# Kernel optimization log

Measured on AMD Instinct MI355X. Metric: run time of the kernel, lower is better.

## Reference

```python
import jax, jax.numpy as jnp
import numpy as np

N_NODES = 50000
N_EDGES = 800000
IN_DIM = 256
HID_DIM = 128
N_LAYERS = 3


def setup_inputs() -> dict:
    key = jax.random.key(0)
    ks = jax.random.split(key, 7)
    s = 0.05
    x = jax.random.normal(ks[0], (N_NODES, IN_DIM), dtype=jnp.float32)
    edge_index = jax.random.randint(ks[1], (2, N_EDGES), 0, N_NODES, dtype=jnp.int64)
    W_enc = jax.random.normal(ks[2], (HID_DIM, IN_DIM), dtype=jnp.float32) * s
    b_enc = jax.random.normal(ks[3], (HID_DIM,), dtype=jnp.float32) * s
    W_l = jax.random.normal(ks[4], (N_LAYERS, HID_DIM, HID_DIM), dtype=jnp.float32) * s
    b_l = jax.random.normal(ks[5], (N_LAYERS, HID_DIM), dtype=jnp.float32) * s
    W_r = jax.random.normal(ks[6], (N_LAYERS, HID_DIM, HID_DIM), dtype=jnp.float32) * s
    return {"x": x, "edge_index": edge_index, "W_enc": W_enc, "b_enc": b_enc,
            "W_l": W_l, "b_l": b_l, "W_r": W_r}


def reference(x, edge_index, W_enc, b_enc, W_l, b_l, W_r):
    # eval mode: dropout is identity
    n = x.shape[0]
    src, dst = edge_index[0], edge_index[1]
    # encode: Linear(in_dim -> hid_dim)
    h = x @ W_enc.T + b_enc  # [N, H]
    # in-degree for mean aggregation (nodes with no in-edges -> 0 output)
    deg = jax.ops.segment_sum(jnp.ones((src.shape[0],), h.dtype), dst, num_segments=n)
    denom = jnp.maximum(deg, 1.0)[:, None]  # [N, 1]
    for i in range(W_l.shape[0]):
        # mean of source-node features over incoming edges
        agg = jax.ops.segment_sum(h[src], dst, num_segments=n) / denom  # [N, H]
        # SAGEConv: lin_l(agg) + lin_r(h)  (lin_r has no bias)
        h = agg @ W_l[i].T + b_l[i] + h @ W_r[i].T
    return h
```

## Files before the change

kernel.cpp:

```cpp
#include <hip/hip_runtime.h>

#define N_NODES 50000
#define N_EDGES 800000
#define IN_DIM 256
#define HID_DIM 128
#define ROWTILES 3125
#define ENC_BLOCKS 1024
#define WCVT_BLOCKS 48
#define CNT_BLOCKS 256
#define EDGES_PER_CB 3125
#define NBLK_LAYER 768
#define CAP_E 352
#define TPAD 3136

typedef float f4 __attribute__((ext_vector_type(4)));
typedef float f32x4 __attribute__((ext_vector_type(4)));
typedef float vf2 __attribute__((ext_vector_type(2)));
typedef short bf16x8 __attribute__((ext_vector_type(8)));

__device__ __forceinline__ unsigned short f2bf(float f) {
    unsigned u = __builtin_bit_cast(unsigned, f);
    return (unsigned short)((u + 0x7fffu + ((u >> 16) & 1u)) >> 16);
}
__device__ __forceinline__ unsigned pk2(float a, float b) {
    return (unsigned)f2bf(a) | ((unsigned)f2bf(b) << 16);
}
__device__ __forceinline__ bf16x8 cvt8(f4 a, f4 b) {
    union { bf16x8 v; unsigned u[4]; } r;
    r.u[0] = pk2(a[0], a[1]);
    r.u[1] = pk2(a[2], a[3]);
    r.u[2] = pk2(b[0], b[1]);
    r.u[3] = pk2(b[2], b[3]);
    return r.v;
}
__device__ __forceinline__ vf2 dec8(unsigned short t) {
    return __builtin_amdgcn_cvt_pk_f32_fp8((int)(unsigned)t, false);
}
__device__ __forceinline__ void gl_lds16(const void* g, void* l) {
    __builtin_amdgcn_global_load_lds(
        (const __attribute__((address_space(1))) unsigned int*)g,
        (__attribute__((address_space(3))) unsigned int*)l, 16, 0, 0);
}


__global__ __launch_bounds__(256) void k_pre(const int* __restrict__ dst,
                                             int* __restrict__ Cm,
                                             const float* __restrict__ Wl, const float* __restrict__ Wr,
                                             unsigned short* __restrict__ wlrbf,
                                             const float* __restrict__ x,
                                             const float* __restrict__ Wenc,
                                             const float* __restrict__ bias,
                                             unsigned short* __restrict__ hout,
                                             unsigned char* __restrict__ f8out) {
    __shared__ int smem_i[8192];
    int tid = threadIdx.x;
    if (blockIdx.x < WCVT_BLOCKS) {
        int idx = blockIdx.x * 2048 + tid * 8;
        const float* srcp = (idx < 49152) ? (Wl + idx) : (Wr + (idx - 49152));
        const f4* g = (const f4*)srcp;
        *(bf16x8*)(wlrbf + idx) = cvt8(g[0], g[1]);
        return;
    }
    if (blockIdx.x >= WCVT_BLOCKS + ENC_BLOCKS) {
        int c = blockIdx.x - WCVT_BLOCKS - ENC_BLOCKS;
        int* cnt = smem_i;
        for (int i = tid; i < TPAD; i += 256) cnt[i] = 0;
        __syncthreads();
        const int* dp = dst + c * EDGES_PER_CB;
        for (int i = tid; i < EDGES_PER_CB; i += 256)
            atomicAdd(&cnt[dp[i] >> 4], 1);
        __syncthreads();
        int* crow = Cm + (size_t)c * TPAD;
        for (int t = tid; t < TPAD; t += 256) crow[t] = cnt[t];
        return;
    }
    float* xsf = (float*)smem_i;
    int bid = blockIdx.x - WCVT_BLOCKS;
    int lane = tid & 63;
    int wv = tid >> 6;
    int colbase = wv * 32;
    int lr = lane & 15;
    int kh = (lane >> 4) * 8;
    int khB = kh * 4;
    int swz = (lr & 7) << 4;

    bf16x8 bfr[2][8];
#pragma unroll
    for (int n = 0; n < 2; ++n) {
        const float* wp = Wenc + (size_t)(colbase + n * 16 + lr) * IN_DIM + kh;
#pragma unroll
        for (int s = 0; s < 8; ++s) {
            const f4* g = (const f4*)(wp + s * 32);
            bfr[n][s] = cvt8(g[0], g[1]);
        }
    }
    float bias0 = bias[colbase + lr];
    float bias1 = bias[colbase + 16 + lr];

    int pb = 0;
    for (int rt = bid; rt < ROWTILES; rt += ENC_BLOCKS, pb ^= 1) {
#pragma unroll
        for (int jj = 0; jj < 4; ++jj) {
            int j = wv * 4 + jj;
            const char* gsrc = (const char*)(x + (size_t)(rt * 16 + j) * IN_DIM)
                               + ((lane * 16) ^ ((j & 7) << 4));
            gl_lds16(gsrc, (char*)(xsf + pb * 4096) + j * 1024);
        }
        __syncthreads();

        const char* xb = (const char*)(xsf + pb * 4096) + lr * 1024;
        bf16x8 afr[8];
#pragma unroll
        for (int s = 0; s < 8; ++s) {
            int lo = khB + s * 128;
            f4 a = *(const f4*)(xb + ((lo) ^ swz));
            f4 b = *(const f4*)(xb + ((lo + 16) ^ swz));
            afr[s] = cvt8(a, b);
        }
        f32x4 acc0 = {0.f, 0.f, 0.f, 0.f}, acc1 = {0.f, 0.f, 0.f, 0.f};
#pragma unroll
        for (int s = 0; s < 8; ++s) {
            acc0 = __builtin_amdgcn_mfma_f32_16x16x32_bf16(afr[s], bfr[0][s], acc0, 0, 0, 0);
            acc1 = __builtin_amdgcn_mfma_f32_16x16x32_bf16(afr[s], bfr[1][s], acc1, 0, 0, 0);
        }
        int rbase = rt * 16 + (lane >> 4) * 4;
#pragma unroll
        for (int r = 0; r < 4; ++r) {
            float v0 = acc0[r] + bias0, v1 = acc1[r] + bias1;
            unsigned short* op = hout + (size_t)(rbase + r) * HID_DIM;
            op[colbase + lr] = f2bf(v0);
            op[colbase + 16 + lr] = f2bf(v1);
            unsigned pk = (unsigned)__builtin_amdgcn_cvt_pk_fp8_f32(v0, v1, 0, false);
            unsigned char* fp = f8out + (size_t)(rbase + r) * HID_DIM;
            fp[colbase + lr] = (unsigned char)(pk & 0xff);
            fp[colbase + 16 + lr] = (unsigned char)((pk >> 8) & 0xff);
        }
    }
}


__global__ __launch_bounds__(256) void k_prefix(const int* __restrict__ Cm,
                                                int* __restrict__ STm,
                                                int* __restrict__ tcnt16) {
    int tid = threadIdx.x;
    int lane = tid & 63;
    int t = blockIdx.x * 4 + (tid >> 6);
    if (t >= ROWTILES) return;
    int b0 = lane * 4;
    int c0 = Cm[(size_t)(b0 + 0) * TPAD + t];
    int c1 = Cm[(size_t)(b0 + 1) * TPAD + t];
    int c2 = Cm[(size_t)(b0 + 2) * TPAD + t];
    int c3 = Cm[(size_t)(b0 + 3) * TPAD + t];
    int ls = c0 + c1 + c2 + c3;
    int incl = ls;
#pragma unroll
    for (int off = 1; off < 64; off <<= 1) {
        int v = __shfl_up(incl, off);
        if (lane >= off) incl += v;
    }
    int excl = incl - ls;
    STm[(size_t)(b0 + 0) * TPAD + t] = excl;
    STm[(size_t)(b0 + 1) * TPAD + t] = excl + c0;
    STm[(size_t)(b0 + 2) * TPAD + t] = excl + c0 + c1;
    STm[(size_t)(b0 + 3) * TPAD + t] = excl + c0 + c1 + c2;
    if (lane == 63) tcnt16[t * 16] = incl;
}


__global__ __launch_bounds__(256) void k_scat(const int* __restrict__ src, const int* __restrict__ dst,
                                              const int* __restrict__ STm,
                                              unsigned* __restrict__ buf) {
    __shared__ int sbase[TPAD];
    __shared__ int lcnt[TPAD];
    int tid = threadIdx.x;
    int c = blockIdx.x;
    const int* strow = STm + (size_t)c * TPAD;
    for (int i = tid; i < TPAD; i += 256) { sbase[i] = strow[i]; lcnt[i] = 0; }
    __syncthreads();
    const int* sp = src + c * EDGES_PER_CB;
    const int* dp = dst + c * EDGES_PER_CB;
    for (int i = tid; i < EDGES_PER_CB; i += 256) {
        int sv = sp[i], dv = dp[i];
        int t = dv >> 4, dl = dv & 15;
        int r = atomicAdd(&lcnt[t], 1);
        int slot = sbase[t] + r;
        if (slot < CAP_E) buf[(size_t)t * CAP_E + slot] = (unsigned)sv | ((unsigned)dl << 16);
    }
}


template <bool LAST>
__global__ __launch_bounds__(256) void k_layer(const unsigned short* __restrict__ H,
                                               const unsigned char* __restrict__ F8,
                                               const int* __restrict__ tcnt16,
                                               const unsigned* __restrict__ buf,
                                               const unsigned short* __restrict__ wlbf,
                                               const unsigned short* __restrict__ wrbf,
                                               const float* __restrict__ bias,
                                               unsigned short* __restrict__ hout,
                                               unsigned char* __restrict__ f8out,
                                               float* __restrict__ fout,
                                               int* __restrict__ ticket) {
    __shared__ unsigned char rowbuf[CAP_E * 128];
    __shared__ unsigned short sorted[CAP_E + 8];
    __shared__ unsigned short aggs[16][136];
    __shared__ int hist[16], pref[17], cur[16];
    __shared__ int tk;
    int tid = threadIdx.x;
    int lane = tid & 63;
    int wv = tid >> 6;
    int colbase = wv * 32;
    int lr = lane & 15;
    int kh = (lane >> 4) * 8;

    bf16x8 bl[2][4], br[2][4];
#pragma unroll
    for (int n = 0; n < 2; ++n) {
        const unsigned short* lp = wlbf + (size_t)(colbase + n * 16 + lr) * HID_DIM + kh;
        const unsigned short* rp = wrbf + (size_t)(colbase + n * 16 + lr) * HID_DIM + kh;
#pragma unroll
        for (int s = 0; s < 4; ++s) {
            bl[n][s] = *(const bf16x8*)(lp + s * 32);
            br[n][s] = *(const bf16x8*)(rp + s * 32);
        }
    }
    float bias0 = bias[colbase + lr];
    float bias1 = bias[colbase + 16 + lr];

    for (;;) {
        if (tid == 0) tk = atomicAdd(ticket, 1);
        if (tid < 16) hist[tid] = 0;
        __syncthreads();
        int rt = tk;
        if (rt >= ROWTILES) break;
        int cnt = tcnt16[rt * 16];
        cnt = (cnt > CAP_E) ? CAP_E : cnt;

        unsigned v0 = 0, v1 = 0;
        bool k0 = tid < cnt, k1 = tid + 256 < cnt;
        if (k0) v0 = buf[(size_t)rt * CAP_E + tid];
        if (k1) v1 = buf[(size_t)rt * CAP_E + tid + 256];
        if (k0) atomicAdd(&hist[v0 >> 16], 1);
        if (k1) atomicAdd(&hist[v1 >> 16], 1);
        __syncthreads();
        if (tid == 0) {
            int acc = 0;
#pragma unroll
            for (int q = 0; q < 16; ++q) { pref[q] = acc; cur[q] = acc; acc += hist[q]; }
            pref[16] = acc;
        }
        __syncthreads();
        if (k0) { int p = atomicAdd(&cur[v0 >> 16], 1); sorted[p] = (unsigned short)(v0 & 0xffff); }
        if (k1) { int p = atomicAdd(&cur[v1 >> 16], 1); sorted[p] = (unsigned short)(v1 & 0xffff); }
        __syncthreads();

        int rb0 = pref[wv * 4] >> 3;
        int rb1 = (pref[wv * 4 + 4] + 7) >> 3;
        for (int i = rb0; i < rb1; ++i) {
            int ee = i * 8 + (lane >> 3);
            ee = (ee > cnt - 1) ? cnt - 1 : ee;
            const unsigned char* gp = F8 + (size_t)sorted[ee] * HID_DIM + (lane & 7) * 16;
            gl_lds16(gp, &rowbuf[i * 1024]);
        }
        asm volatile("s_waitcnt vmcnt(0)" ::: "memory");
        __builtin_amdgcn_sched_barrier(0);

#pragma unroll
        for (int q = 0; q < 4; ++q) {
            int nq = wv * 4 + q;
            int jb = pref[nq], je = pref[nq + 1];
            float a0 = 0.f, a1 = 0.f;
            int j = jb;
            for (; j + 4 <= je; j += 4) {
                unsigned short t0 = *(const unsigned short*)&rowbuf[(j + 0) * 128 + lane * 2];
                unsigned short t1 = *(const unsigned short*)&rowbuf[(j + 1) * 128 + lane * 2];
                unsigned short t2 = *(const unsigned short*)&rowbuf[(j + 2) * 128 + lane * 2];
                unsigned short t3 = *(const unsigned short*)&rowbuf[(j + 3) * 128 + lane * 2];
                vf2 f0 = dec8(t0), f1 = dec8(t1), f2_ = dec8(t2), f3 = dec8(t3);
                a0 += (f0[0] + f1[0]) + (f2_[0] + f3[0]);
                a1 += (f0[1] + f1[1]) + (f2_[1] + f3[1]);
            }
            for (; j < je; ++j) {
                unsigned short t0 = *(const unsigned short*)&rowbuf[j * 128 + lane * 2];
                vf2 f0 = dec8(t0);
                a0 += f0[0];
                a1 += f0[1];
            }
            int dg = je - jb;
            float inv = 1.0f / (float)(dg > 0 ? dg : 1);
            *(unsigned*)&aggs[nq][lane * 2] = pk2(a0 * inv, a1 * inv);
        }
        __syncthreads();

        bf16x8 afr[4], hfr[4];
        const unsigned short* hp = H + (size_t)(rt * 16 + lr) * HID_DIM + kh;
#pragma unroll
        for (int s = 0; s < 4; ++s) {
            afr[s] = *(const bf16x8*)&aggs[lr][kh + s * 32];
            hfr[s] = *(const bf16x8*)(hp + s * 32);
        }
        f32x4 acc0 = {0.f, 0.f, 0.f, 0.f}, acc1 = {0.f, 0.f, 0.f, 0.f};
#pragma unroll
        for (int s = 0; s < 4; ++s) {
            acc0 = __builtin_amdgcn_mfma_f32_16x16x32_bf16(afr[s], bl[0][s], acc0, 0, 0, 0);
            acc1 = __builtin_amdgcn_mfma_f32_16x16x32_bf16(afr[s], bl[1][s], acc1, 0, 0, 0);
            acc0 = __builtin_amdgcn_mfma_f32_16x16x32_bf16(hfr[s], br[0][s], acc0, 0, 0, 0);
            acc1 = __builtin_amdgcn_mfma_f32_16x16x32_bf16(hfr[s], br[1][s], acc1, 0, 0, 0);
        }
        int rbase = rt * 16 + (lane >> 4) * 4;
#pragma unroll
        for (int r = 0; r < 4; ++r) {
            float v0 = acc0[r] + bias0, v1 = acc1[r] + bias1;
            if (LAST) {
                float* op = fout + (size_t)(rbase + r) * HID_DIM;
                op[colbase + lr] = v0;
                op[colbase + 16 + lr] = v1;
            } else {
                unsigned short* op = hout + (size_t)(rbase + r) * HID_DIM;
                op[colbase + lr] = f2bf(v0);
                op[colbase + 16 + lr] = f2bf(v1);
                unsigned pk = (unsigned)__builtin_amdgcn_cvt_pk_fp8_f32(v0, v1, 0, false);
                unsigned char* fp = f8out + (size_t)(rbase + r) * HID_DIM;
                fp[colbase + lr] = (unsigned char)(pk & 0xff);
                fp[colbase + 16 + lr] = (unsigned char)((pk >> 8) & 0xff);
            }
        }
    }
}


extern "C" void kernel_launch(void* const* d_in, const int* in_sizes, int n_in,
                              void* d_out, int out_size, void* d_ws, size_t ws_size,
                              hipStream_t stream) {
    const float* x    = (const float*)d_in[0];
    const int*   ei   = (const int*)d_in[1];
    const float* Wenc = (const float*)d_in[2];
    const float* benc = (const float*)d_in[3];
    const float* Wl   = (const float*)d_in[4];
    const float* bl   = (const float*)d_in[5];
    const float* Wr   = (const float*)d_in[6];
    float* out = (float*)d_out;

    const int* srcv = ei;
    const int* dstv = ei + N_EDGES;

    char* p = (char*)d_ws;
    unsigned short* h0    = (unsigned short*)p; p += (size_t)N_NODES * HID_DIM * 2;
    unsigned short* h1    = (unsigned short*)p; p += (size_t)N_NODES * HID_DIM * 2;
    unsigned char*  h0f   = (unsigned char*)p;  p += (size_t)N_NODES * HID_DIM;
    unsigned char*  h1f   = (unsigned char*)p;  p += (size_t)N_NODES * HID_DIM;
    unsigned short* wlrbf = (unsigned short*)p; p += 98304 * 2;
    int*      tcnt16 = (int*)p;      p += 3136 * 16 * 4;
    int*      tick   = (int*)p;      p += 256;
    unsigned* buf    = (unsigned*)p; p += (size_t)ROWTILES * CAP_E * 4;

    int* Cm  = (int*)h1;
    int* STm = (int*)((char*)h1 + (size_t)CNT_BLOCKS * TPAD * 4);

    unsigned short* wlbf = wlrbf;
    unsigned short* wrbf = wlrbf + 49152;

    (void)hipMemsetAsync(tcnt16, 0, 3136 * 16 * 4 + 256, stream);
    k_pre<<<WCVT_BLOCKS + ENC_BLOCKS + CNT_BLOCKS, 256, 0, stream>>>(
        dstv, Cm, Wl, Wr, wlrbf, x, Wenc, benc, h0, h0f);
    k_prefix<<<(ROWTILES + 3) / 4, 256, 0, stream>>>(Cm, STm, tcnt16);
    k_scat<<<CNT_BLOCKS, 256, 0, stream>>>(srcv, dstv, STm, buf);

    k_layer<false><<<NBLK_LAYER, 256, 0, stream>>>(h0, h0f, tcnt16, buf, wlbf, wrbf, bl,
                                                   h1, h1f, nullptr, tick + 1);
    k_layer<false><<<NBLK_LAYER, 256, 0, stream>>>(h1, h1f, tcnt16, buf, wlbf + 16384, wrbf + 16384,
                                                   bl + HID_DIM, h0, h0f, nullptr, tick + 2);
    k_layer<true><<<NBLK_LAYER, 256, 0, stream>>>(h0, h0f, tcnt16, buf, wlbf + 32768, wrbf + 32768,
                                                  bl + 2 * HID_DIM, nullptr, nullptr, out, tick + 3);
}
```

Measured before the change: 215.1 us.

## Presort per-tile edge lists once and prefetch next tile in layer kernels

Adds a k_sort2 kernel that buckets each 16-row tile's edges by destination row once, storing sorted source ids and per-row prefix offsets. The three layer kernels previously redid this histogram/scatter sort with several block barriers on every tile. The layer kernels now take a static grid stride instead of an atomic ticket, with the block count raised. They double-buffer the next tile's ids and prefixes and issue the H fragment loads early to overlap latency. In exchange there is an extra kernel launch, extra workspace traffic for the sorted ids, and the memset of counters and tickets is dropped.

```diff
diff --git a/kernel.cpp b/kernel.cpp
--- a/kernel.cpp
+++ b/kernel.cpp
@@ -9,7 +9,7 @@
 #define WCVT_BLOCKS 48
 #define CNT_BLOCKS 256
 #define EDGES_PER_CB 3125
-#define NBLK_LAYER 768
+#define NBLK_LAYER 1563
 #define CAP_E 352
 #define TPAD 3136
 
@@ -189,23 +189,70 @@
 }
 
 
+__global__ __launch_bounds__(256) void k_sort2(const unsigned* __restrict__ buf,
+                                               const int* __restrict__ tcnt16,
+                                               unsigned short* __restrict__ idg,
+                                               unsigned short* __restrict__ preft) {
+    __shared__ unsigned short stmp[4][512];
+    __shared__ int hcur[4][32];
+    int tid = threadIdx.x, lane = tid & 63, w = tid >> 6;
+    int t = blockIdx.x * 4 + w;
+    bool act = t < ROWTILES;
+    int cnt = 0;
+    if (act) { cnt = tcnt16[t * 16]; if (cnt > CAP_E) cnt = CAP_E; }
+    if (lane < 32) hcur[w][lane] = 0;
+    unsigned ev[6];
+#pragma unroll
+    for (int k = 0; k < 6; ++k) {
+        int i = lane + k * 64;
+        ev[k] = (act && i < cnt) ? buf[(size_t)t * CAP_E + i] : 0xFFFFFFFFu;
+    }
+    __syncthreads();
+#pragma unroll
+    for (int k = 0; k < 6; ++k)
+        if (ev[k] != 0xFFFFFFFFu) atomicAdd(&hcur[w][ev[k] >> 16], 1);
+    __syncthreads();
+    int hv = (lane < 16) ? hcur[w][lane] : 0;
+    int incl = hv;
+#pragma unroll
+    for (int off = 1; off <= 16; off <<= 1) {
+        int v = __shfl_up(incl, off);
+        if (lane >= off) incl += v;
+    }
+    int excl = incl - hv;
+    if (act && lane < 16) hcur[w][16 + lane] = excl;
+    if (act && lane <= 16) preft[(size_t)t * 32 + lane] = (unsigned short)excl;
+    __syncthreads();
+#pragma unroll
+    for (int k = 0; k < 6; ++k)
+        if (ev[k] != 0xFFFFFFFFu) {
+            int r = atomicAdd(&hcur[w][16 + (ev[k] >> 16)], 1);
+            stmp[w][r] = (unsigned short)(ev[k] & 0xffff);
+        }
+    __syncthreads();
+    if (act) {
+        unsigned* op = (unsigned*)(idg + (size_t)t * 512);
+        const unsigned* ip = (const unsigned*)stmp[w];
+        int nu = (cnt + 1) >> 1;
+        for (int i = lane; i < nu; i += 64) op[i] = ip[i];
+    }
+}
+
+
 template <bool LAST>
 __global__ __launch_bounds__(256) void k_layer(const unsigned short* __restrict__ H,
                                                const unsigned char* __restrict__ F8,
-                                               const int* __restrict__ tcnt16,
-                                               const unsigned* __restrict__ buf,
+                                               const unsigned short* __restrict__ idg,
+                                               const unsigned short* __restrict__ preft,
                                                const unsigned short* __restrict__ wlbf,
                                                const unsigned short* __restrict__ wrbf,
                                                const float* __restrict__ bias,
                                                unsigned short* __restrict__ hout,
                                                unsigned char* __restrict__ f8out,
-                                               float* __restrict__ fout,
-                                               int* __restrict__ ticket) {
+                                               float* __restrict__ fout) {
     __shared__ unsigned char rowbuf[CAP_E * 128];
-    __shared__ unsigned short sorted[CAP_E + 8];
     __shared__ unsigned short aggs[16][136];
-    __shared__ int hist[16], pref[17], cur[16];
-    __shared__ int tk;
+    __shared__ unsigned short idsb[2][512];
     int tid = threadIdx.x;
     int lane = tid & 63;
     int wv = tid >> 6;
@@ -227,40 +274,33 @@
     float bias0 = bias[colbase + lr];
     float bias1 = bias[colbase + 16 + lr];
 
-    for (;;) {
-        if (tid == 0) tk = atomicAdd(ticket, 1);
-        if (tid < 16) hist[tid] = 0;
-        __syncthreads();
-        int rt = tk;
-        if (rt >= ROWTILES) break;
-        int cnt = tcnt16[rt * 16];
-        cnt = (cnt > CAP_E) ? CAP_E : cnt;
-
-        unsigned v0 = 0, v1 = 0;
-        bool k0 = tid < cnt, k1 = tid + 256 < cnt;
-        if (k0) v0 = buf[(size_t)rt * CAP_E + tid];
-        if (k1) v1 = buf[(size_t)rt * CAP_E + tid + 256];
-        if (k0) atomicAdd(&hist[v0 >> 16], 1);
-        if (k1) atomicAdd(&hist[v1 >> 16], 1);
-        __syncthreads();
-        if (tid == 0) {
-            int acc = 0;
-#pragma unroll
-            for (int q = 0; q < 16; ++q) { pref[q] = acc; cur[q] = acc; acc += hist[q]; }
-            pref[16] = acc;
-        }
-        __syncthreads();
-        if (k0) { int p = atomicAdd(&cur[v0 >> 16], 1); sorted[p] = (unsigned short)(v0 & 0xffff); }
-        if (k1) { int p = atomicAdd(&cur[v1 >> 16], 1); sorted[p] = (unsigned short)(v1 & 0xffff); }
-        __syncthreads();
-
-        int rb0 = pref[wv * 4] >> 3;
-        int rb1 = (pref[wv * 4 + 4] + 7) >> 3;
+    int rt0 = blockIdx.x;
+    gl_lds16((const char*)(idg + (size_t)rt0 * 512) + lane * 16, (void*)idsb[0]);
+    int pc = (int)preft[(size_t)rt0 * 32 + (lane < 16 ? lane : 16)];
+    asm volatile("s_waitcnt vmcnt(0)" ::: "memory");
+    __builtin_amdgcn_sched_barrier(0);
+
+    int pb = 0;
+    for (int rt = rt0; rt < ROWTILES; rt += NBLK_LAYER, pb ^= 1) {
+        int cnt = __shfl(pc, 16);
+        int rb0 = __shfl(pc, wv * 4) >> 3;
+        int rb1 = (__shfl(pc, wv * 4 + 4) + 7) >> 3;
+
         for (int i = rb0; i < rb1; ++i) {
             int ee = i * 8 + (lane >> 3);
             ee = (ee > cnt - 1) ? cnt - 1 : ee;
-            const unsigned char* gp = F8 + (size_t)sorted[ee] * HID_DIM + (lane & 7) * 16;
+            const unsigned char* gp = F8 + (size_t)idsb[pb][ee] * HID_DIM + (lane & 7) * 16;
             gl_lds16(gp, &rowbuf[i * 1024]);
+        }
+        const unsigned short* hp = H + (size_t)(rt * 16 + lr) * HID_DIM + kh;
+        bf16x8 hfr[4];
+#pragma unroll
+        for (int s = 0; s < 4; ++s) hfr[s] = *(const bf16x8*)(hp + s * 32);
+        int rtn = rt + NBLK_LAYER;
+        int pn = 0;
+        if (rtn < ROWTILES) {
+            gl_lds16((const char*)(idg + (size_t)rtn * 512) + lane * 16, (void*)idsb[pb ^ 1]);
+            pn = (int)preft[(size_t)rtn * 32 + (lane < 16 ? lane : 16)];
         }
         asm volatile("s_waitcnt vmcnt(0)" ::: "memory");
         __builtin_amdgcn_sched_barrier(0);
@@ -268,7 +308,7 @@
 #pragma unroll
         for (int q = 0; q < 4; ++q) {
             int nq = wv * 4 + q;
-            int jb = pref[nq], je = pref[nq + 1];
+            int jb = __shfl(pc, nq), je = __shfl(pc, nq + 1);
             float a0 = 0.f, a1 = 0.f;
             int j = jb;
             for (; j + 4 <= je; j += 4) {
@@ -292,13 +332,9 @@
         }
         __syncthreads();
 
-        bf16x8 afr[4], hfr[4];
-        const unsigned short* hp = H + (size_t)(rt * 16 + lr) * HID_DIM + kh;
-#pragma unroll
-        for (int s = 0; s < 4; ++s) {
-            afr[s] = *(const bf16x8*)&aggs[lr][kh + s * 32];
-            hfr[s] = *(const bf16x8*)(hp + s * 32);
-        }
+        bf16x8 afr[4];
+#pragma unroll
+        for (int s = 0; s < 4; ++s) afr[s] = *(const bf16x8*)&aggs[lr][kh + s * 32];
         f32x4 acc0 = {0.f, 0.f, 0.f, 0.f}, acc1 = {0.f, 0.f, 0.f, 0.f};
 #pragma unroll
         for (int s = 0; s < 4; ++s) {
@@ -325,6 +361,8 @@
                 fp[colbase + 16 + lr] = (unsigned char)((pk >> 8) & 0xff);
             }
         }
+        __syncthreads();
+        pc = pn;
     }
 }
 
@@ -351,7 +389,8 @@
     unsigned char*  h1f   = (unsigned char*)p;  p += (size_t)N_NODES * HID_DIM;
     unsigned short* wlrbf = (unsigned short*)p; p += 98304 * 2;
     int*      tcnt16 = (int*)p;      p += 3136 * 16 * 4;
-    int*      tick   = (int*)p;      p += 256;
+    unsigned short* idg   = (unsigned short*)p; p += (size_t)ROWTILES * 512 * 2;
+    unsigned short* preft = (unsigned short*)p; p += (size_t)ROWTILES * 32 * 2;
     unsigned* buf    = (unsigned*)p; p += (size_t)ROWTILES * CAP_E * 4;
 
     int* Cm  = (int*)h1;
@@ -360,16 +399,16 @@
     unsigned short* wlbf = wlrbf;
     unsigned short* wrbf = wlrbf + 49152;
 
-    (void)hipMemsetAsync(tcnt16, 0, 3136 * 16 * 4 + 256, stream);
     k_pre<<<WCVT_BLOCKS + ENC_BLOCKS + CNT_BLOCKS, 256, 0, stream>>>(
         dstv, Cm, Wl, Wr, wlrbf, x, Wenc, benc, h0, h0f);
     k_prefix<<<(ROWTILES + 3) / 4, 256, 0, stream>>>(Cm, STm, tcnt16);
     k_scat<<<CNT_BLOCKS, 256, 0, stream>>>(srcv, dstv, STm, buf);
-
-    k_layer<false><<<NBLK_LAYER, 256, 0, stream>>>(h0, h0f, tcnt16, buf, wlbf, wrbf, bl,
-                                                   h1, h1f, nullptr, tick + 1);
-    k_layer<false><<<NBLK_LAYER, 256, 0, stream>>>(h1, h1f, tcnt16, buf, wlbf + 16384, wrbf + 16384,
-                                                   bl + HID_DIM, h0, h0f, nullptr, tick + 2);
-    k_layer<true><<<NBLK_LAYER, 256, 0, stream>>>(h0, h0f, tcnt16, buf, wlbf + 32768, wrbf + 32768,
-                                                  bl + 2 * HID_DIM, nullptr, nullptr, out, tick + 3);
-}
+    k_sort2<<<(ROWTILES + 3) / 4, 256, 0, stream>>>(buf, tcnt16, idg, preft);
+
+    k_layer<false><<<NBLK_LAYER, 256, 0, stream>>>(h0, h0f, idg, preft, wlbf, wrbf, bl,
+                                                   h1, h1f, nullptr);
+    k_layer<false><<<NBLK_LAYER, 256, 0, stream>>>(h1, h1f, idg, preft, wlbf + 16384, wrbf + 16384,
+                                                   bl + HID_DIM, h0, h0f, nullptr);
+    k_layer<true><<<NBLK_LAYER, 256, 0, stream>>>(h0, h0f, idg, preft, wlbf + 32768, wrbf + 32768,
+                                                  bl + 2 * HID_DIM, nullptr, nullptr, out);
+}
```

After: 179.0 us. -16.8%, faster.
